# Kernel optimization log

Measured on AMD Instinct MI355X. Metric: run time of the kernel, lower is better.

The kernel has to match this reference:

```python
import jax, jax.numpy as jnp
import numpy as np

N_U, N_V = 8000, 8000
E_U, E_V = 128000, 128000
ND, ED, T = 40, 10, 3


def _lin(key, out_d, in_d):
    k1, k2 = jax.random.split(key)
    s = 1.0 / np.sqrt(in_d)
    w = jax.random.uniform(k1, (out_d, in_d), minval=-s, maxval=s, dtype=jnp.float32)
    b = jax.random.uniform(k2, (out_d,), minval=-s, maxval=s, dtype=jnp.float32)
    return w, b


def _lstm(key, in_d, h_d):
    ks = jax.random.split(key, 4)
    s = 1.0 / np.sqrt(h_d)
    Wih = jax.random.uniform(ks[0], (4 * h_d, in_d), minval=-s, maxval=s, dtype=jnp.float32)
    Whh = jax.random.uniform(ks[1], (4 * h_d, h_d), minval=-s, maxval=s, dtype=jnp.float32)
    bih = jax.random.uniform(ks[2], (4 * h_d,), minval=-s, maxval=s, dtype=jnp.float32)
    bhh = jax.random.uniform(ks[3], (4 * h_d,), minval=-s, maxval=s, dtype=jnp.float32)
    return Wih, Whh, bih, bhh


def _mp_params(key):
    ks = jax.random.split(key, 2 * T)
    Uw, Ub, Mw, Mb = [], [], [], []
    for k in range(T):
        w, b = _lin(ks[2 * k], ND, 2 * ND + ED); Uw.append(w); Ub.append(b)
        w, b = _lin(ks[2 * k + 1], ND, 2 * ND); Mw.append(w); Mb.append(b)
    return jnp.stack(Uw), jnp.stack(Ub), jnp.stack(Mw), jnp.stack(Mb)


def setup_inputs():
    key = jax.random.key(0)
    ks = jax.random.split(key, 20)
    d = {}
    d["nodes_u"] = jax.random.normal(ks[0], (N_U, ND), jnp.float32)
    d["ei_u"] = jax.random.randint(ks[1], (2, E_U), 0, N_U)
    d["ef_u"] = jax.random.normal(ks[2], (E_U, ED), jnp.float32)
    d["nodes_v"] = jax.random.normal(ks[3], (N_V, ND), jnp.float32)
    d["ei_v"] = jax.random.randint(ks[4], (2, E_V), 0, N_V)
    d["ef_v"] = jax.random.normal(ks[5], (E_V, ED), jnp.float32)
    d["Uw_u"], d["Ub_u"], d["Mw_u"], d["Mb_u"] = _mp_params(ks[6])
    d["Uw_v"], d["Ub_v"], d["Mw_v"], d["Mb_v"] = _mp_params(ks[7])
    d["ls_Wih"], d["ls_Whh"], d["ls_bih"], d["ls_bhh"] = _lstm(ks[8], 2 * ND, ND)
    d["lv_Wih"], d["lv_Whh"], d["lv_bih"], d["lv_bhh"] = _lstm(ks[9], 2 * ND, ND)
    d["gs_Wih"], d["gs_Whh"], d["gs_bih"], d["gs_bhh"] = _lstm(ks[10], 8 * ND, 4 * ND)
    d["gv_Wih"], d["gv_Whh"], d["gv_bih"], d["gv_bhh"] = _lstm(ks[11], 8 * ND, 4 * ND)
    d["w1"], d["b1"] = _lin(ks[12], 360, 16 * ND)
    d["w2"], d["b2"] = _lin(ks[13], 200, 360)
    d["w3"], d["b3"] = _lin(ks[14], 120, 200)
    d["w4"], d["b4"] = _lin(ks[15], 1, 120)
    return d


def _lstm_step(x, h, c, Wih, Whh, bih, bhh):
    # one seq_len=1 step of torch nn.LSTM; gate order i, f, g, o
    gates = x @ Wih.T + h @ Whh.T + bih + bhh
    i, f, g, o = jnp.split(gates, 4, axis=-1)
    c = jax.nn.sigmoid(f) * c + jax.nn.sigmoid(i) * jnp.tanh(g)
    h = jax.nn.sigmoid(o) * jnp.tanh(c)
    return h, c


def _message_passing(h, ei, ef, Uw, Ub, Mw, Mb):
    # vectorized form of the per-node Python loop: messages use the
    # pre-update h each round (the torch code computes all messages first).
    src, dst = ei[0], ei[1]
    n = h.shape[0]
    for k in range(T):
        z = jnp.concatenate([h[src], h[dst], ef], axis=-1)   # [E, 2*ND+ED]
        msg_e = z @ Uw[k].T + Ub[k]                          # [E, ND]
        msg = jax.ops.segment_sum(msg_e, src, num_segments=n)
        h = jax.nn.relu(jnp.concatenate([h, msg], axis=-1) @ Mw[k].T + Mb[k])
    return h


def _set2set_pair(h0, ht, Wih, Whh, bih, bhh, steps=2):
    # set of size 2 ({h_0, h_T}) per node; nodes act as the LSTM batch.
    t = jnp.stack([h0, ht], axis=0)                # [2, n, f]
    n, f = h0.shape
    q_star = jnp.zeros((n, 2 * f), h0.dtype)
    h = jnp.zeros((n, f), h0.dtype)
    c = jnp.zeros((n, f), h0.dtype)
    for _ in range(steps):
        h, c = _lstm_step(q_star, h, c, Wih, Whh, bih, bhh)
        e = jnp.sum(t * h[None], axis=2)           # [2, n]
        a = jax.nn.softmax(e, axis=0)
        r = jnp.sum(a[..., None] * t, axis=0)      # [n, f]
        q_star = jnp.concatenate([h, r], axis=1)
    return q_star                                   # [n, 2f]


def _set2set_pool(x, Wih, Whh, bih, bhh, steps=2):
    # attention pooling over nodes, batch of 1 (the gather set2set).
    n, f = x.shape
    q_star = jnp.zeros((1, 2 * f), x.dtype)
    h = jnp.zeros((1, f), x.dtype)
    c = jnp.zeros((1, f), x.dtype)
    for _ in range(steps):
        h, c = _lstm_step(q_star, h, c, Wih, Whh, bih, bhh)
        a = jax.nn.softmax(x @ h[0])                # [n]
        r = (a[:, None] * x).sum(axis=0, keepdims=True)
        q_star = jnp.concatenate([h, r], axis=1)
    return q_star                                    # [1, 2f]


def reference(nodes_u, ei_u, ef_u, nodes_v, ei_v, ef_v,
              Uw_u, Ub_u, Mw_u, Mb_u, Uw_v, Ub_v, Mw_v, Mb_v,
              ls_Wih, ls_Whh, ls_bih, ls_bhh,
              lv_Wih, lv_Whh, lv_bih, lv_bhh,
              gs_Wih, gs_Whh, gs_bih, gs_bhh,
              gv_Wih, gv_Whh, gv_bih, gv_bhh,
              w1, b1, w2, b2, w3, b3, w4, b4):
    hu_t = _message_passing(nodes_u, ei_u, ef_u, Uw_u, Ub_u, Mw_u, Mb_u)
    hv_t = _message_passing(nodes_v, ei_v, ef_v, Uw_v, Ub_v, Mw_v, Mb_v)
    gu = _set2set_pair(nodes_u, hu_t, ls_Wih, ls_Whh, ls_bih, ls_bhh)  # [n, 2*ND]
    gv = _set2set_pair(nodes_v, hv_t, lv_Wih, lv_Whh, lv_bih, lv_bhh)  # [m, 2*ND]
    interaction = gu @ gv.T                          # [n, m]
    im2 = jnp.tanh(interaction)
    u_after = im2 @ gv                               # [n, 2*ND]
    v_after = im2.T @ gu                             # [m, 2*ND]
    cu = _set2set_pool(jnp.concatenate([u_after, gu], 1), gs_Wih, gs_Whh, gs_bih, gs_bhh)
    cv = _set2set_pool(jnp.concatenate([v_after, gv], 1), gv_Wih, gv_Whh, gv_bih, gv_bhh)
    x = jnp.concatenate([cu, cv], axis=1)            # [1, 16*ND]
    x = jax.nn.relu(x @ w1.T + b1)
    x = jax.nn.relu(x @ w2.T + b2)
    x = jax.nn.relu(x @ w3.T + b3)
    x = x @ w4.T + b4                                # [1, 1]
    return (x, interaction)
```

## Files before the change

kernel.cpp:

```cpp
#include <hip/hip_runtime.h>
#include <cstdint>
#include <cstddef>

#define NN 8000
#define NE 128000
#define NDv 40
#define EDv 10

typedef __attribute__((ext_vector_type(8))) short short8v;
typedef __attribute__((ext_vector_type(4))) float f32x4;

__device__ __forceinline__ float rcp_fast(float x) { return __builtin_amdgcn_rcpf(x); }
__device__ __forceinline__ float sigm(float x) { return rcp_fast(1.f + __expf(-x)); }
__device__ __forceinline__ float ftanh(float x) {
    float e = __expf(2.f * x);
    return 1.f - 2.f * rcp_fast(e + 1.f);
}
__device__ __forceinline__ short f2bf(float x) {
    unsigned u = __builtin_bit_cast(unsigned, x);
    u += 0x7fffu + ((u >> 16) & 1u);
    return (short)(u >> 16);
}
__device__ __forceinline__ float wsum(float v) {
    for (int o = 32; o; o >>= 1) v += __shfl_down(v, o);
    return v;
}
__device__ __forceinline__ float wmax(float v) {
    for (int o = 32; o; o >>= 1) v = fmaxf(v, __shfl_down(v, o));
    return v;
}


__global__ __launch_bounds__(256) void csr_deg2_kernel(const int* __restrict__ ei_u, const int* __restrict__ ei_v,
                                                       int* __restrict__ deg_u, int* __restrict__ deg_v) {
    const int* ei = blockIdx.y ? ei_v : ei_u;
    int* deg = blockIdx.y ? deg_v : deg_u;
    int e = blockIdx.x * 256 + threadIdx.x;
    if (e < NE) atomicAdd(&deg[ei[e]], 1);
}

__global__ __launch_bounds__(256) void sef2_kernel(const int* __restrict__ ei_u, const int* __restrict__ ei_v,
                                                   const float* __restrict__ ef_u, const float* __restrict__ ef_v,
                                                   float* __restrict__ sef_u, float* __restrict__ sef_v) {
    const int* ei = blockIdx.y ? ei_v : ei_u;
    const float* ef = blockIdx.y ? ef_v : ef_u;
    float* sef = blockIdx.y ? sef_v : sef_u;
    int t = blockIdx.x * 256 + threadIdx.x;
    int e = t / EDv, k = t % EDv;
    atomicAdd(&sef[ei[e] * EDv + k], ef[t]);
}

__global__ __launch_bounds__(64) void csr_scan2_kernel(const int* __restrict__ deg_u, const int* __restrict__ deg_v,
                                                       int* __restrict__ off_u, int* __restrict__ off_v,
                                                       int* __restrict__ woff_u, int* __restrict__ woff_v) {
    const int* deg = blockIdx.x ? deg_v : deg_u;
    int* off = blockIdx.x ? off_v : off_u;
    int* woff = blockIdx.x ? woff_v : woff_u;
    int l = threadIdx.x;
    int base = l * 125;
    int s = 0;
    for (int i = 0; i < 125; ++i) s += deg[base + i];
    int pre = s;
    for (int o = 1; o < 64; o <<= 1) { int t = __shfl_up(pre, o); if (l >= o) pre += t; }
    pre -= s;
    int run = pre;
    for (int i = 0; i < 125; ++i) {
        off[base + i] = run; woff[base + i] = run;
        run += deg[base + i];
    }
    if (l == 63) off[NN] = run;
}

__global__ __launch_bounds__(256) void csr_fill2_kernel(const int* __restrict__ ei_u, const int* __restrict__ ei_v,
                                                        int* __restrict__ woff_u, int* __restrict__ woff_v,
                                                        int* __restrict__ dl_u, int* __restrict__ dl_v) {
    const int* ei = blockIdx.y ? ei_v : ei_u;
    int* woff = blockIdx.y ? woff_v : woff_u;
    int* dlist = blockIdx.y ? dl_v : dl_u;
    int e = blockIdx.x * 256 + threadIdx.x;
    if (e < NE) { int p = atomicAdd(&woff[ei[e]], 1); dlist[p] = ei[NE + e]; }
}


__global__ __launch_bounds__(256) void node_proj2_kernel(const float* __restrict__ h_u, const float* __restrict__ h_v,
                                                         const float* __restrict__ Uw_u, const float* __restrict__ Uw_v,
                                                         float* __restrict__ A_u, float* __restrict__ B_u,
                                                         float* __restrict__ A_v, float* __restrict__ B_v) {
    const float* h = blockIdx.y ? h_v : h_u;
    const float* Uw = blockIdx.y ? Uw_v : Uw_u;
    float* A = blockIdx.y ? A_v : A_u;
    float* B = blockIdx.y ? B_v : B_u;
    __shared__ float W[40][81];
    int tid = threadIdx.x;
    for (int s = tid; s < 3200; s += 256) W[s / 80][s % 80] = Uw[(s / 80) * 90 + (s % 80)];
    __syncthreads();
    int t = blockIdx.x * 256 + tid;
    int n = t / NDv, i = t % NDv;
    float hreg[40];
    const float* hr = h + n * NDv;
#pragma unroll
    for (int k4 = 0; k4 < 10; ++k4) {
        float4 v = *reinterpret_cast<const float4*>(hr + k4 * 4);
        hreg[k4 * 4 + 0] = v.x; hreg[k4 * 4 + 1] = v.y; hreg[k4 * 4 + 2] = v.z; hreg[k4 * 4 + 3] = v.w;
    }
    float a = 0.f, b = 0.f;
#pragma unroll
    for (int k = 0; k < NDv; ++k) { a += W[i][k] * hreg[k]; b += W[i][40 + k] * hreg[k]; }
    A[t] = a; B[t] = b;
}

__global__ __launch_bounds__(320) void mp_round2_kernel(
    const int* __restrict__ off_u, const int* __restrict__ dl_u, const float* __restrict__ sef_u,
    const float* __restrict__ UwE_u, const float* __restrict__ Ub_u,
    const float* __restrict__ Mw_u, const float* __restrict__ Mb_u, const float* __restrict__ UwN_u,
    const float* __restrict__ h_u, const float* __restrict__ A_u, const float* __restrict__ B_u,
    float* __restrict__ hout_u, float* __restrict__ Ao_u, float* __restrict__ Bo_u,
    const int* __restrict__ off_v, const int* __restrict__ dl_v, const float* __restrict__ sef_v,
    const float* __restrict__ UwE_v, const float* __restrict__ Ub_v,
    const float* __restrict__ Mw_v, const float* __restrict__ Mb_v, const float* __restrict__ UwN_v,
    const float* __restrict__ h_v, const float* __restrict__ A_v, const float* __restrict__ B_v,
    float* __restrict__ hout_v, float* __restrict__ Ao_v, float* __restrict__ Bo_v,
    int has_next) {
    const int* off = blockIdx.y ? off_v : off_u;
    const int* dlist = blockIdx.y ? dl_v : dl_u;
    const float* sef = blockIdx.y ? sef_v : sef_u;
    const float* UwE = blockIdx.y ? UwE_v : UwE_u;
    const float* Ub = blockIdx.y ? Ub_v : Ub_u;
    const float* Mw = blockIdx.y ? Mw_v : Mw_u;
    const float* Mb = blockIdx.y ? Mb_v : Mb_u;
    const float* UwN = blockIdx.y ? UwN_v : UwN_u;
    const float* h = blockIdx.y ? h_v : h_u;
    const float* A = blockIdx.y ? A_v : A_u;
    const float* B = blockIdx.y ? B_v : B_u;
    float* hout = blockIdx.y ? hout_v : hout_u;
    float* Ao = blockIdx.y ? Ao_v : Ao_u;
    float* Bo = blockIdx.y ? Bo_v : Bo_u;

    __shared__ float WM[40][81];
    __shared__ float WU[40][81];
    __shared__ float msgS[8][40];
    __shared__ float hS[8][41];
    __shared__ float houtS[8][41];

    int tid = threadIdx.x;
    for (int s = tid; s < 3200; s += 320) WM[s / 80][s % 80] = Mw[s];
    if (has_next)
        for (int s = tid; s < 3200; s += 320) WU[s / 80][s % 80] = UwN[(s / 80) * 90 + (s % 80)];
    int ln = tid / NDv, i = tid % NDv;
    int n = blockIdx.x * 8 + ln;
    int t = n * NDv + i;
    hS[ln][i] = h[t];

    const float* we = UwE + i * 90 + 80;
    const float* se = sef + n * EDv;
    int p0 = off[n], p1 = off[n + 1];
    float acc = (float)(p1 - p0) * (A[t] + Ub[i]);
#pragma unroll
    for (int k = 0; k < EDv; ++k) acc += we[k] * se[k];
    for (int p = p0; p < p1; ++p) acc += B[dlist[p] * NDv + i];
    msgS[ln][i] = acc;
    __syncthreads();

    float a2 = Mb[i];
#pragma unroll
    for (int k = 0; k < NDv; ++k) a2 += WM[i][k] * hS[ln][k];
#pragma unroll
    for (int k = 0; k < NDv; ++k) a2 += WM[i][40 + k] * msgS[ln][k];
    float ho = fmaxf(a2, 0.f);
    hout[t] = ho;
    if (has_next) {
        houtS[ln][i] = ho;
        __syncthreads();
        float a = 0.f, b = 0.f;
#pragma unroll
        for (int k = 0; k < NDv; ++k) { float hv = houtS[ln][k]; a += WU[i][k] * hv; b += WU[i][40 + k] * hv; }
        Ao[t] = a; Bo[t] = b;
    }
}


__global__ __launch_bounds__(64) void s2s_init2_kernel(const float* __restrict__ bih_u, const float* __restrict__ bhh_u,
                                                       const float* __restrict__ bih_v, const float* __restrict__ bhh_v,
                                                       float* __restrict__ h1_u, float* __restrict__ c1_u,
                                                       float* __restrict__ h1_v, float* __restrict__ c1_v) {
    const float* bih = blockIdx.y ? bih_v : bih_u;
    const float* bhh = blockIdx.y ? bhh_v : bhh_u;
    float* h1 = blockIdx.y ? h1_v : h1_u;
    float* c1 = blockIdx.y ? c1_v : c1_u;
    int i = threadIdx.x;
    if (i < 40) {
        float gi = bih[i] + bhh[i];
        float gg = bih[80 + i] + bhh[80 + i];
        float go = bih[120 + i] + bhh[120 + i];
        float c = sigm(gi) * ftanh(gg);
        c1[i] = c;
        h1[i] = sigm(go) * ftanh(c);
    }
}

__global__ __launch_bounds__(256) void s2s_step0_kernel(const float* __restrict__ h0_u, const float* __restrict__ ht_u,
                                                        const float* __restrict__ h1_u, float* __restrict__ q_u,
                                                        float* __restrict__ rT_u,
                                                        const float* __restrict__ h0_v, const float* __restrict__ ht_v,
                                                        const float* __restrict__ h1_v, float* __restrict__ q_v,
                                                        float* __restrict__ rT_v) {
    const float* h0 = blockIdx.y ? h0_v : h0_u;
    const float* ht = blockIdx.y ? ht_v : ht_u;
    const float* h1 = blockIdx.y ? h1_v : h1_u;
    float* q = blockIdx.y ? q_v : q_u;
    float* rT = blockIdx.y ? rT_v : rT_u;
    int tid = threadIdx.x;
    int nl = tid >> 2, lg = tid & 3;
    int n = blockIdx.x * 64 + nl;
    float h0r[10], htr[10];
    float e0 = 0.f, e1 = 0.f;
#pragma unroll
    for (int k = 0; k < 10; ++k) {
        int i = lg * 10 + k;
        h0r[k] = h0[n * 40 + i];
        htr[k] = ht[n * 40 + i];
        float hv = h1[i];
        e0 += h0r[k] * hv;
        e1 += htr[k] * hv;
    }
    e0 += __shfl_xor(e0, 1); e0 += __shfl_xor(e0, 2);
    e1 += __shfl_xor(e1, 1); e1 += __shfl_xor(e1, 2);
    float m = fmaxf(e0, e1);
    float p0 = __expf(e0 - m), p1 = __expf(e1 - m);
    float inv = rcp_fast(p0 + p1);
    float a0 = p0 * inv, a1 = p1 * inv;
#pragma unroll
    for (int k = 0; k < 10; ++k) {
        int i = lg * 10 + k;
        float r = a0 * h0r[k] + a1 * htr[k];
        q[n * 80 + i] = h1[i];
        q[n * 80 + 40 + i] = r;
        rT[i * NN + n] = r;
    }
}

__global__ __launch_bounds__(64) void s2s_base2_kernel(const float* __restrict__ Wih_u, const float* __restrict__ Whh_u,
                                                       const float* __restrict__ bih_u, const float* __restrict__ bhh_u,
                                                       const float* __restrict__ h1_u,
                                                       const float* __restrict__ Wih_v, const float* __restrict__ Whh_v,
                                                       const float* __restrict__ bih_v, const float* __restrict__ bhh_v,
                                                       const float* __restrict__ h1_v,
                                                       float* __restrict__ base2) {
    const float* Wih = blockIdx.y ? Wih_v : Wih_u;
    const float* Whh = blockIdx.y ? Whh_v : Whh_u;
    const float* bih = blockIdx.y ? bih_v : bih_u;
    const float* bhh = blockIdx.y ? bhh_v : bhh_u;
    const float* h1 = blockIdx.y ? h1_v : h1_u;
    int j = blockIdx.x;
    int lane = threadIdx.x;
    float p = 0.f;
    if (lane < 40) p = (Wih[j * 80 + lane] + Whh[j * 40 + lane]) * h1[lane];
    p = wsum(p);
    if (lane == 0) base2[blockIdx.y * 160 + j] = p + bih[j] + bhh[j];
}

__global__ __launch_bounds__(256) void s2s_gates1_kernel(const float* __restrict__ rT_u, const float* __restrict__ Wih_u,
                                                         float* __restrict__ gT_u,
                                                         const float* __restrict__ rT_v, const float* __restrict__ Wih_v,
                                                         float* __restrict__ gT_v,
                                                         const float* __restrict__ base2) {
    const float* rT = blockIdx.y ? rT_v : rT_u;
    const float* Wih = blockIdx.y ? Wih_v : Wih_u;
    float* gatesT = blockIdx.y ? gT_v : gT_u;
    const float* base = base2 + blockIdx.y * 160;
    int t = blockIdx.x * 256 + threadIdx.x;
    int n = t % NN;
    int jg = t / NN;
    float rr[40];
#pragma unroll
    for (int k = 0; k < 40; ++k) rr[k] = rT[k * NN + n];
#pragma unroll
    for (int jj = 0; jj < 8; ++jj) {
        int j = jg * 8 + jj;
        const float* wi = Wih + j * 80 + 40;
        float acc = base[j];
#pragma unroll
        for (int k = 0; k < 40; ++k) acc += wi[k] * rr[k];
        gatesT[j * NN + n] = acc;
    }
}

__global__ __launch_bounds__(256) void s2s_upd1_kernel(const float* __restrict__ gT_u, const float* __restrict__ h0_u,
                                                       const float* __restrict__ ht_u, const float* __restrict__ c1_u,
                                                       float* __restrict__ q_u,
                                                       const float* __restrict__ gT_v, const float* __restrict__ h0_v,
                                                       const float* __restrict__ ht_v, const float* __restrict__ c1_v,
                                                       float* __restrict__ q_v) {
    const float* gT = blockIdx.y ? gT_v : gT_u;
    const float* h0 = blockIdx.y ? h0_v : h0_u;
    const float* ht = blockIdx.y ? ht_v : ht_u;
    const float* c1 = blockIdx.y ? c1_v : c1_u;
    float* q = blockIdx.y ? q_v : q_u;
    int tid = threadIdx.x;
    int nl = tid >> 2, lg = tid & 3;
    int n = blockIdx.x * 64 + nl;
    float h0r[10], htr[10], hnr[10];
    float e0 = 0.f, e1 = 0.f;
#pragma unroll
    for (int k = 0; k < 10; ++k) {
        int i = lg * 10 + k;
        float gi = gT[i * NN + n];
        float gf = gT[(40 + i) * NN + n];
        float gg = gT[(80 + i) * NN + n];
        float go = gT[(120 + i) * NN + n];
        float cn = sigm(gf) * c1[i] + sigm(gi) * ftanh(gg);
        float hn = sigm(go) * ftanh(cn);
        hnr[k] = hn;
        h0r[k] = h0[n * 40 + i];
        htr[k] = ht[n * 40 + i];
        e0 += h0r[k] * hn;
        e1 += htr[k] * hn;
    }
    e0 += __shfl_xor(e0, 1); e0 += __shfl_xor(e0, 2);
    e1 += __shfl_xor(e1, 1); e1 += __shfl_xor(e1, 2);
    float m = fmaxf(e0, e1);
    float p0 = __expf(e0 - m), p1 = __expf(e1 - m);
    float inv = rcp_fast(p0 + p1);
    float a0 = p0 * inv, a1 = p1 * inv;
#pragma unroll
    for (int k = 0; k < 10; ++k) {
        int i = lg * 10 + k;
        q[n * 80 + i] = hnr[k];
        q[n * 80 + 40 + i] = a0 * h0r[k] + a1 * htr[k];
    }
}


__global__ __launch_bounds__(256) void cast_all_kernel(const float* __restrict__ gu, const float* __restrict__ gv,
                                                       short* __restrict__ ouT, short* __restrict__ ovT,
                                                       short* __restrict__ oub, short* __restrict__ ovb,
                                                       float* __restrict__ qTu, float* __restrict__ qTv) {
    const float* g = blockIdx.y ? gv : gu;
    if (blockIdx.x < 2500) {
        short* o = blockIdx.y ? ovT : ouT;
        float* qT = blockIdx.y ? qTv : qTu;
        int t = blockIdx.x * 256 + threadIdx.x;
        int m = t % NN, f = t / NN;
        float val = g[m * 80 + f];
        o[t] = f2bf(val);
        qT[t] = val;
    } else {
        short* o = blockIdx.y ? ovb : oub;
        int t = (blockIdx.x - 2500) * 256 + threadIdx.x;
        int m = t / 96, k = t % 96;
        o[t] = (k < 80) ? f2bf(g[m * 80 + k]) : (short)0;
    }
}


__global__ __launch_bounds__(256, 2) void fused_kernel(const short* __restrict__ gub, const short* __restrict__ gvb,
                                                       const short* __restrict__ guT, const short* __restrict__ gvT,
                                                       float* __restrict__ inter,
                                                       float* __restrict__ uafT, float* __restrict__ vafT) {
    __shared__ short P[4][16][72];
    const short* Xb; const short* Yb; const short* YT; float* afT;
    bool storeI = (blockIdx.z == 0);
    if (storeI) { Xb = gub; Yb = gvb; YT = gvT; afT = uafT; }
    else        { Xb = gvb; Yb = gub; YT = guT; afT = vafT; }
    int tid = threadIdx.x;
    int w = tid >> 6, l = tid & 63;
    int lrow = l & 15, lk = l >> 4;
    int x0 = blockIdx.x * 64;
    int it0 = (125 * blockIdx.y) >> 1;
    int it1 = (125 * (blockIdx.y + 1)) >> 1;
    short8v a_x[3];
    const short* arow = Xb + (size_t)(x0 + w * 16 + lrow) * 96 + lk * 8;
#pragma unroll
    for (int ks = 0; ks < 3; ++ks) a_x[ks] = *reinterpret_cast<const short8v*>(arow + ks * 32);
    const short* ybase = Yb + (size_t)lrow * 96 + lk * 8;

    f32x4 acc[5] = {};
    short8v bc[12], bn[12];
#pragma unroll
    for (int i = 0; i < 12; ++i) {
        int ks = i >> 2, nt = i & 3;
        bc[i] = *reinterpret_cast<const short8v*>(ybase + (size_t)(it0 * 64 + nt * 16) * 96 + ks * 32);
    }
    for (int it = it0; it < it1; ++it) {
        int k0 = it * 64;
        if (it + 1 < it1) {
#pragma unroll
            for (int i = 0; i < 12; ++i) {
                int ks = i >> 2, nt = i & 3;
                bn[i] = *reinterpret_cast<const short8v*>(ybase + (size_t)(k0 + 64 + nt * 16) * 96 + ks * 32);
            }
        }
        short8v byt[10];
#pragma unroll
        for (int ks2 = 0; ks2 < 2; ++ks2)
#pragma unroll
            for (int ft = 0; ft < 5; ++ft)
                byt[ks2 * 5 + ft] = *reinterpret_cast<const short8v*>(YT + (size_t)(ft * 16 + lrow) * NN + k0 + ks2 * 32 + lk * 8);
        f32x4 accI[4] = {};
#pragma unroll
        for (int ks = 0; ks < 3; ++ks)
#pragma unroll
            for (int nt = 0; nt < 4; ++nt)
                accI[nt] = __builtin_amdgcn_mfma_f32_16x16x32_bf16(a_x[ks], bc[ks * 4 + nt], accI[nt], 0, 0, 0);
#pragma unroll
        for (int nt = 0; nt < 4; ++nt)
#pragma unroll
            for (int r = 0; r < 4; ++r)
                P[w][lk * 4 + r][nt * 16 + lrow] = f2bf(ftanh(accI[nt][r]));
#pragma unroll
        for (int ks2 = 0; ks2 < 2; ++ks2) {
            short8v ap = *reinterpret_cast<const short8v*>(&P[w][lrow][ks2 * 32 + lk * 8]);
#pragma unroll
            for (int ft = 0; ft < 5; ++ft)
                acc[ft] = __builtin_amdgcn_mfma_f32_16x16x32_bf16(ap, byt[ks2 * 5 + ft], acc[ft], 0, 0, 0);
        }
        if (storeI) {
#pragma unroll
            for (int nt = 0; nt < 4; ++nt)
#pragma unroll
                for (int r = 0; r < 4; ++r)
                    inter[(size_t)(x0 + w * 16 + lk * 4 + r) * NN + (k0 + nt * 16 + lrow)] = accI[nt][r];
        }
#pragma unroll
        for (int i = 0; i < 12; ++i) bc[i] = bn[i];
    }
    int xout = x0 + w * 16 + lk * 4;
#pragma unroll
    for (int ft = 0; ft < 5; ++ft)
#pragma unroll
        for (int r = 0; r < 4; ++r)
            atomicAdd(&afT[(size_t)(ft * 16 + lrow) * NN + xout + r], acc[ft][r]);
}


__global__ __launch_bounds__(256) void pool_init2_kernel(const float* __restrict__ bih_u, const float* __restrict__ bhh_u,
                                                         const float* __restrict__ bih_v, const float* __restrict__ bhh_v,
                                                         float* __restrict__ ph_u, float* __restrict__ pc_u,
                                                         float* __restrict__ pq_u,
                                                         float* __restrict__ ph_v, float* __restrict__ pc_v,
                                                         float* __restrict__ pq_v) {
    const float* bih = blockIdx.y ? bih_v : bih_u;
    const float* bhh = blockIdx.y ? bhh_v : bhh_u;
    float* ph = blockIdx.y ? ph_v : ph_u;
    float* pc = blockIdx.y ? pc_v : pc_u;
    float* pq = blockIdx.y ? pq_v : pq_u;
    int i = threadIdx.x;
    if (i < 160) {
        float gi = bih[i] + bhh[i];
        float gg = bih[320 + i] + bhh[320 + i];
        float go = bih[480 + i] + bhh[480 + i];
        float c = sigm(gi) * ftanh(gg);
        pc[i] = c;
        float h = sigm(go) * ftanh(c);
        ph[i] = h;
        pq[i] = h;
    }
}

__global__ __launch_bounds__(64) void gates_pool2_kernel(const float* __restrict__ Wih_u, const float* __restrict__ Whh_u,
                                                         const float* __restrict__ bih_u, const float* __restrict__ bhh_u,
                                                         const float* __restrict__ q_u, const float* __restrict__ h_u,
                                                         const float* __restrict__ Wih_v, const float* __restrict__ Whh_v,
                                                         const float* __restrict__ bih_v, const float* __restrict__ bhh_v,
                                                         const float* __restrict__ q_v, const float* __restrict__ h_v,
                                                         float* __restrict__ gts2) {
    const float* Wih = blockIdx.y ? Wih_v : Wih_u;
    const float* Whh = blockIdx.y ? Whh_v : Whh_u;
    const float* bih = blockIdx.y ? bih_v : bih_u;
    const float* bhh = blockIdx.y ? bhh_v : bhh_u;
    const float* q = blockIdx.y ? q_v : q_u;
    const float* h = blockIdx.y ? h_v : h_u;
    float* gts = gts2 + blockIdx.y * 640;
    int j = blockIdx.x;
    int lane = threadIdx.x;
    const float* wi = Wih + j * 320;
    const float* wh = Whh + j * 160;
    float p = 0.f;
#pragma unroll
    for (int k4 = 0; k4 < 5; ++k4) { int k = lane + k4 * 64; p += wi[k] * q[k]; }
#pragma unroll
    for (int k4 = 0; k4 < 3; ++k4) { int k = lane + k4 * 64; if (k < 160) p += wh[k] * h[k]; }
    p = wsum(p);
    if (lane == 0) gts[j] = p + bih[j] + bhh[j];
}

__global__ __launch_bounds__(256) void pool_point2_kernel(const float* __restrict__ gts2,
                                                          float* __restrict__ h_u, float* __restrict__ c_u,
                                                          float* __restrict__ q_u,
                                                          float* __restrict__ h_v, float* __restrict__ c_v,
                                                          float* __restrict__ q_v) {
    const float* gts = gts2 + blockIdx.y * 640;
    float* h = blockIdx.y ? h_v : h_u;
    float* c = blockIdx.y ? c_v : c_u;
    float* q = blockIdx.y ? q_v : q_u;
    int tid = threadIdx.x;
    if (tid < 160) {
        float cn = sigm(gts[160 + tid]) * c[tid] + sigm(gts[tid]) * ftanh(gts[320 + tid]);
        c[tid] = cn;
        float hn = sigm(gts[480 + tid]) * ftanh(cn);
        h[tid] = hn;
        q[tid] = hn;
    }
}

__global__ __launch_bounds__(256) void pool_scores2_kernel(const float* __restrict__ uafT, const float* __restrict__ qTu,
                                                           const float* __restrict__ h_u, float* __restrict__ sc_u,
                                                           const float* __restrict__ vafT, const float* __restrict__ qTv,
                                                           const float* __restrict__ h_v, float* __restrict__ sc_v,
                                                           float* __restrict__ pmax2) {
    const float* afT = blockIdx.y ? vafT : uafT;
    const float* qT = blockIdx.y ? qTv : qTu;
    const float* h = blockIdx.y ? h_v : h_u;
    float* scores = blockIdx.y ? sc_v : sc_u;
    float* pmax = pmax2 + blockIdx.y * 32;
    int tid = threadIdx.x;
    int n = blockIdx.x * 256 + tid;
    float s = -3.4e38f;
    if (n < NN) {
        float acc = 0.f;
#pragma unroll 8
        for (int k = 0; k < 80; ++k) acc += afT[k * NN + n] * h[k];
#pragma unroll 8
        for (int k = 0; k < 80; ++k) acc += qT[k * NN + n] * h[80 + k];
        scores[n] = acc;
        s = acc;
    }
    __shared__ float red[4];
    float m = wmax(s);
    if ((tid & 63) == 0) red[tid >> 6] = m;
    __syncthreads();
    if (tid == 0) pmax[blockIdx.x] = fmaxf(fmaxf(red[0], red[1]), fmaxf(red[2], red[3]));
}

__global__ __launch_bounds__(256) void pool_r2_kernel(const float* __restrict__ uafT, const float* __restrict__ qTu,
                                                      const float* __restrict__ sc_u,
                                                      const float* __restrict__ vafT, const float* __restrict__ qTv,
                                                      const float* __restrict__ sc_v,
                                                      const float* __restrict__ pmax2,
                                                      float* __restrict__ pq_u, float* __restrict__ pq_v) {
    const float* afT = blockIdx.y ? vafT : uafT;
    const float* qT = blockIdx.y ? qTv : qTu;
    const float* scores = blockIdx.y ? sc_v : sc_u;
    float* q = blockIdx.y ? pq_v : pq_u;
    const float* pmax = pmax2 + blockIdx.y * 32;
    int f = blockIdx.x;
    int tid = threadIdx.x;
    __shared__ float smax;
    __shared__ float reda[4], redd[4];
    if (tid < 64) {
        float m = (tid < 32) ? pmax[tid] : -3.4e38f;
        m = wmax(m);
        if (tid == 0) smax = m;
    }
    __syncthreads();
    float m = smax;
    const float* x = (f < 80) ? (afT + (size_t)f * NN) : (qT + (size_t)(f - 80) * NN);
    float acc = 0.f, den = 0.f;
    for (int n = tid; n < NN; n += 256) { float e = __expf(scores[n] - m); den += e; acc += e * x[n]; }
    float wa = wsum(acc), wd = wsum(den);
    if ((tid & 63) == 0) { reda[tid >> 6] = wa; redd[tid >> 6] = wd; }
    __syncthreads();
    if (tid == 0) {
        float A = reda[0] + reda[1] + reda[2] + reda[3];
        float D = redd[0] + redd[1] + redd[2] + redd[3];
        q[160 + f] = A * rcp_fast(D);
    }
}


__global__ __launch_bounds__(64) void gemv_kernel(const float* __restrict__ W, const float* __restrict__ b,
                                                  const float* __restrict__ x, float* __restrict__ y,
                                                  int K, int relu) {
    int j = blockIdx.x;
    int lane = threadIdx.x;
    const float* w = W + (size_t)j * K;
    float p = 0.f;
    for (int k = lane; k < K; k += 64) p += w[k] * x[k];
    p = wsum(p);
    if (lane == 0) {
        p += b[j];
        y[j] = relu ? fmaxf(p, 0.f) : p;
    }
}


extern "C" void kernel_launch(void* const* d_in, const int* in_sizes, int n_in,
                              void* d_out, int out_size, void* d_ws, size_t ws_size,
                              hipStream_t stream) {
    const float* nodes_u = (const float*)d_in[0];
    const int* ei_u = (const int*)d_in[1];
    const float* ef_u = (const float*)d_in[2];
    const float* nodes_v = (const float*)d_in[3];
    const int* ei_v = (const int*)d_in[4];
    const float* ef_v = (const float*)d_in[5];
    const float* Uw_u = (const float*)d_in[6];
    const float* Ub_u = (const float*)d_in[7];
    const float* Mw_u = (const float*)d_in[8];
    const float* Mb_u = (const float*)d_in[9];
    const float* Uw_v = (const float*)d_in[10];
    const float* Ub_v = (const float*)d_in[11];
    const float* Mw_v = (const float*)d_in[12];
    const float* Mb_v = (const float*)d_in[13];
    const float* lsWih = (const float*)d_in[14];
    const float* lsWhh = (const float*)d_in[15];
    const float* lsbih = (const float*)d_in[16];
    const float* lsbhh = (const float*)d_in[17];
    const float* lvWih = (const float*)d_in[18];
    const float* lvWhh = (const float*)d_in[19];
    const float* lvbih = (const float*)d_in[20];
    const float* lvbhh = (const float*)d_in[21];
    const float* gsWih = (const float*)d_in[22];
    const float* gsWhh = (const float*)d_in[23];
    const float* gsbih = (const float*)d_in[24];
    const float* gsbhh = (const float*)d_in[25];
    const float* gvWih = (const float*)d_in[26];
    const float* gvWhh = (const float*)d_in[27];
    const float* gvbih = (const float*)d_in[28];
    const float* gvbhh = (const float*)d_in[29];
    const float* w1 = (const float*)d_in[30];
    const float* b1 = (const float*)d_in[31];
    const float* w2 = (const float*)d_in[32];
    const float* b2 = (const float*)d_in[33];
    const float* w3 = (const float*)d_in[34];
    const float* b3 = (const float*)d_in[35];
    const float* w4 = (const float*)d_in[36];
    const float* b4 = (const float*)d_in[37];

    float* ws = (float*)d_ws;
    float* hA_u = ws + 0;
    float* hB_u = ws + 320000;
    float* hA_v = ws + 640000;
    float* hB_v = ws + 960000;
    float* A0_u = ws + 1600000;
    float* B0_u = ws + 1920000;
    float* q_u  = ws + 2240000;
    float* q_v  = ws + 2880000;
    float* A1_u = ws + 2240000;
    float* B1_u = ws + 2560000;
    float* A1_v = ws + 2880000;
    float* B1_v = ws + 3200000;
    float* sef_u = ws + 4160000;
    float* sef_v = ws + 4240000;
    float* gT_u = ws + 4160000;
    float* gT_v = ws + 5440000;
    float* uafT = ws + 5440000;
    float* vafT = ws + 6080000;
    float* rT_u = ws + 1600000;
    float* rT_v = ws + 1920000;
    float* qT_u = ws + 1600000;
    float* qT_v = ws + 2240000;
    float* sc_u = ws + 6720000;
    float* sc_v = ws + 6728000;
    float* pmax2 = ws + 6736000;
    float* pq_u = ws + 6736080;
    float* pq_v = ws + 6736400;
    float* ph_u = ws + 6736720;
    float* pc_u = ws + 6736880;
    float* ph_v = ws + 6737040;
    float* pc_v = ws + 6737200;
    float* pgts2 = ws + 6737360;
    float* mx1  = ws + 6738640;
    float* mx2  = ws + 6739000;
    float* mx3  = ws + 6739200;
    float* h1_u = ws + 6739320;
    float* c1_u = ws + 6739360;
    float* h1_v = ws + 6739400;
    float* c1_v = ws + 6739440;
    float* base2 = ws + 6739480;
    int* ioff_u   = (int*)(ws + 6740000);
    int* idlist_u = (int*)(ws + 6748064);
    int* ioff_v   = (int*)(ws + 6876064);
    int* idlist_v = (int*)(ws + 6884128);
    int* iwoff_u  = (int*)(ws + 7012128);
    int* ideg_u   = (int*)(ws + 7020192);
    int* iwoff_v  = (int*)(ws + 7028256);
    int* ideg_v   = (int*)(ws + 7036320);
    float* A0_v = ws + 7339536;
    float* B0_v = ws + 7659536;

    short* guT = (short*)(ws + 0);
    short* gvT = (short*)(ws + 320000);
    short* gub = (short*)(ws + 640000);
    short* gvb = (short*)(ws + 1024000);

    float* out = (float*)d_out;
    float* inter = out + 1;

    hipMemsetAsync(ideg_u, 0, (7044384 - 7020192) * sizeof(int), stream);
    hipMemsetAsync(sef_u, 0, 2 * NN * EDv * sizeof(float), stream);
    csr_deg2_kernel<<<dim3(500, 2), 256, 0, stream>>>(ei_u, ei_v, ideg_u, ideg_v);
    csr_scan2_kernel<<<2, 64, 0, stream>>>(ideg_u, ideg_v, ioff_u, ioff_v, iwoff_u, iwoff_v);
    csr_fill2_kernel<<<dim3(500, 2), 256, 0, stream>>>(ei_u, ei_v, iwoff_u, iwoff_v, idlist_u, idlist_v);
    sef2_kernel<<<dim3(5000, 2), 256, 0, stream>>>(ei_u, ei_v, ef_u, ef_v, sef_u, sef_v);

    node_proj2_kernel<<<dim3(1250, 2), 256, 0, stream>>>(nodes_u, nodes_v, Uw_u, Uw_v, A0_u, B0_u, A0_v, B0_v);
    mp_round2_kernel<<<dim3(1000, 2), 320, 0, stream>>>(
        ioff_u, idlist_u, sef_u, Uw_u, Ub_u, Mw_u, Mb_u, Uw_u + 3600,
        nodes_u, A0_u, B0_u, hA_u, A1_u, B1_u,
        ioff_v, idlist_v, sef_v, Uw_v, Ub_v, Mw_v, Mb_v, Uw_v + 3600,
        nodes_v, A0_v, B0_v, hA_v, A1_v, B1_v, 1);
    mp_round2_kernel<<<dim3(1000, 2), 320, 0, stream>>>(
        ioff_u, idlist_u, sef_u, Uw_u + 3600, Ub_u + 40, Mw_u + 3200, Mb_u + 40, Uw_u + 7200,
        hA_u, A1_u, B1_u, hB_u, A0_u, B0_u,
        ioff_v, idlist_v, sef_v, Uw_v + 3600, Ub_v + 40, Mw_v + 3200, Mb_v + 40, Uw_v + 7200,
        hA_v, A1_v, B1_v, hB_v, A0_v, B0_v, 1);
    mp_round2_kernel<<<dim3(1000, 2), 320, 0, stream>>>(
        ioff_u, idlist_u, sef_u, Uw_u + 7200, Ub_u + 80, Mw_u + 6400, Mb_u + 80, nullptr,
        hB_u, A0_u, B0_u, hA_u, nullptr, nullptr,
        ioff_v, idlist_v, sef_v, Uw_v + 7200, Ub_v + 80, Mw_v + 6400, Mb_v + 80, nullptr,
        hB_v, A0_v, B0_v, hA_v, nullptr, nullptr, 0);

    s2s_init2_kernel<<<dim3(1, 2), 64, 0, stream>>>(lsbih, lsbhh, lvbih, lvbhh, h1_u, c1_u, h1_v, c1_v);
    s2s_step0_kernel<<<dim3(125, 2), 256, 0, stream>>>(nodes_u, hA_u, h1_u, q_u, rT_u,
                                                       nodes_v, hA_v, h1_v, q_v, rT_v);
    s2s_base2_kernel<<<dim3(160, 2), 64, 0, stream>>>(lsWih, lsWhh, lsbih, lsbhh, h1_u,
                                                      lvWih, lvWhh, lvbih, lvbhh, h1_v, base2);
    s2s_gates1_kernel<<<dim3(625, 2), 256, 0, stream>>>(rT_u, lsWih, gT_u, rT_v, lvWih, gT_v, base2);
    s2s_upd1_kernel<<<dim3(125, 2), 256, 0, stream>>>(gT_u, nodes_u, hA_u, c1_u, q_u,
                                                      gT_v, nodes_v, hA_v, c1_v, q_v);

    cast_all_kernel<<<dim3(5500, 2), 256, 0, stream>>>(q_u, q_v, guT, gvT, gub, gvb, qT_u, qT_v);

    hipMemsetAsync(uafT, 0, 1280000 * sizeof(float), stream);
    fused_kernel<<<dim3(125, 2, 2), 256, 0, stream>>>(gub, gvb, guT, gvT, inter, uafT, vafT);

    pool_init2_kernel<<<dim3(1, 2), 256, 0, stream>>>(gsbih, gsbhh, gvbih, gvbhh,
                                                      ph_u, pc_u, pq_u, ph_v, pc_v, pq_v);
    pool_scores2_kernel<<<dim3(32, 2), 256, 0, stream>>>(uafT, qT_u, ph_u, sc_u, vafT, qT_v, ph_v, sc_v, pmax2);
    pool_r2_kernel<<<dim3(160, 2), 256, 0, stream>>>(uafT, qT_u, sc_u, vafT, qT_v, sc_v, pmax2, pq_u, pq_v);
    gates_pool2_kernel<<<dim3(640, 2), 64, 0, stream>>>(gsWih, gsWhh, gsbih, gsbhh, pq_u, ph_u,
                                                        gvWih, gvWhh, gvbih, gvbhh, pq_v, ph_v, pgts2);
    pool_point2_kernel<<<dim3(1, 2), 256, 0, stream>>>(pgts2, ph_u, pc_u, pq_u, ph_v, pc_v, pq_v);
    pool_scores2_kernel<<<dim3(32, 2), 256, 0, stream>>>(uafT, qT_u, ph_u, sc_u, vafT, qT_v, ph_v, sc_v, pmax2);
    pool_r2_kernel<<<dim3(160, 2), 256, 0, stream>>>(uafT, qT_u, sc_u, vafT, qT_v, sc_v, pmax2, pq_u, pq_v);

    gemv_kernel<<<360, 64, 0, stream>>>(w1, b1, pq_u, mx1, 640, 1);
    gemv_kernel<<<200, 64, 0, stream>>>(w2, b2, mx1, mx2, 360, 1);
    gemv_kernel<<<120, 64, 0, stream>>>(w3, b3, mx2, mx3, 200, 1);
    gemv_kernel<<<1, 64, 0, stream>>>(w4, b4, mx3, out, 120, 0);
}
```

Before: 635.6 us.

## Fuse set2set gate GEMV into LSTM update, enlarge MP blocks, unsplit fused grid

```diff
diff --git a/kernel.cpp b/kernel.cpp
--- a/kernel.cpp
+++ b/kernel.cpp
@@ -109,7 +109,7 @@
     A[t] = a; B[t] = b;
 }
 
-__global__ __launch_bounds__(320) void mp_round2_kernel(
+__global__ __launch_bounds__(640) void mp_round2_kernel(
     const int* __restrict__ off_u, const int* __restrict__ dl_u, const float* __restrict__ sef_u,
     const float* __restrict__ UwE_u, const float* __restrict__ Ub_u,
     const float* __restrict__ Mw_u, const float* __restrict__ Mb_u, const float* __restrict__ UwN_u,
@@ -138,16 +138,16 @@
 
     __shared__ float WM[40][81];
     __shared__ float WU[40][81];
-    __shared__ float msgS[8][40];
-    __shared__ float hS[8][41];
-    __shared__ float houtS[8][41];
+    __shared__ float msgS[16][40];
+    __shared__ float hS[16][41];
+    __shared__ float houtS[16][41];
 
     int tid = threadIdx.x;
-    for (int s = tid; s < 3200; s += 320) WM[s / 80][s % 80] = Mw[s];
+    for (int s = tid; s < 3200; s += 640) WM[s / 80][s % 80] = Mw[s];
     if (has_next)
-        for (int s = tid; s < 3200; s += 320) WU[s / 80][s % 80] = UwN[(s / 80) * 90 + (s % 80)];
+        for (int s = tid; s < 3200; s += 640) WU[s / 80][s % 80] = UwN[(s / 80) * 90 + (s % 80)];
     int ln = tid / NDv, i = tid % NDv;
-    int n = blockIdx.x * 8 + ln;
+    int n = blockIdx.x * 16 + ln;
     int t = n * NDv + i;
     hS[ln][i] = h[t];
 
@@ -259,57 +259,45 @@
     if (lane == 0) base2[blockIdx.y * 160 + j] = p + bih[j] + bhh[j];
 }
 
-__global__ __launch_bounds__(256) void s2s_gates1_kernel(const float* __restrict__ rT_u, const float* __restrict__ Wih_u,
-                                                         float* __restrict__ gT_u,
-                                                         const float* __restrict__ rT_v, const float* __restrict__ Wih_v,
-                                                         float* __restrict__ gT_v,
-                                                         const float* __restrict__ base2) {
+__global__ __launch_bounds__(256) void s2s_step1_kernel(const float* __restrict__ rT_u, const float* __restrict__ Wih_u,
+                                                        const float* __restrict__ h0_u, const float* __restrict__ ht_u,
+                                                        const float* __restrict__ c1_u, float* __restrict__ q_u,
+                                                        const float* __restrict__ rT_v, const float* __restrict__ Wih_v,
+                                                        const float* __restrict__ h0_v, const float* __restrict__ ht_v,
+                                                        const float* __restrict__ c1_v, float* __restrict__ q_v,
+                                                        const float* __restrict__ base2) {
     const float* rT = blockIdx.y ? rT_v : rT_u;
     const float* Wih = blockIdx.y ? Wih_v : Wih_u;
-    float* gatesT = blockIdx.y ? gT_v : gT_u;
-    const float* base = base2 + blockIdx.y * 160;
-    int t = blockIdx.x * 256 + threadIdx.x;
-    int n = t % NN;
-    int jg = t / NN;
-    float rr[40];
-#pragma unroll
-    for (int k = 0; k < 40; ++k) rr[k] = rT[k * NN + n];
-#pragma unroll
-    for (int jj = 0; jj < 8; ++jj) {
-        int j = jg * 8 + jj;
-        const float* wi = Wih + j * 80 + 40;
-        float acc = base[j];
-#pragma unroll
-        for (int k = 0; k < 40; ++k) acc += wi[k] * rr[k];
-        gatesT[j * NN + n] = acc;
-    }
-}
-
-__global__ __launch_bounds__(256) void s2s_upd1_kernel(const float* __restrict__ gT_u, const float* __restrict__ h0_u,
-                                                       const float* __restrict__ ht_u, const float* __restrict__ c1_u,
-                                                       float* __restrict__ q_u,
-                                                       const float* __restrict__ gT_v, const float* __restrict__ h0_v,
-                                                       const float* __restrict__ ht_v, const float* __restrict__ c1_v,
-                                                       float* __restrict__ q_v) {
-    const float* gT = blockIdx.y ? gT_v : gT_u;
     const float* h0 = blockIdx.y ? h0_v : h0_u;
     const float* ht = blockIdx.y ? ht_v : ht_u;
     const float* c1 = blockIdx.y ? c1_v : c1_u;
     float* q = blockIdx.y ? q_v : q_u;
+    const float* base = base2 + blockIdx.y * 160;
     int tid = threadIdx.x;
     int nl = tid >> 2, lg = tid & 3;
     int n = blockIdx.x * 64 + nl;
+    float rr[40];
+#pragma unroll
+    for (int k = 0; k < 40; ++k) rr[k] = rT[k * NN + n];
+    float g[40];
+#pragma unroll
+    for (int gq = 0; gq < 4; ++gq)
+#pragma unroll
+        for (int k = 0; k < 10; ++k) {
+            int j = gq * 40 + lg * 10 + k;
+            const float* wi = Wih + j * 80 + 40;
+            float acc = base[j];
+#pragma unroll
+            for (int kk = 0; kk < 40; ++kk) acc += wi[kk] * rr[kk];
+            g[gq * 10 + k] = acc;
+        }
     float h0r[10], htr[10], hnr[10];
     float e0 = 0.f, e1 = 0.f;
 #pragma unroll
     for (int k = 0; k < 10; ++k) {
         int i = lg * 10 + k;
-        float gi = gT[i * NN + n];
-        float gf = gT[(40 + i) * NN + n];
-        float gg = gT[(80 + i) * NN + n];
-        float go = gT[(120 + i) * NN + n];
-        float cn = sigm(gf) * c1[i] + sigm(gi) * ftanh(gg);
-        float hn = sigm(go) * ftanh(cn);
+        float cn = sigm(g[10 + k]) * c1[i] + sigm(g[k]) * ftanh(g[20 + k]);
+        float hn = sigm(g[30 + k]) * ftanh(cn);
         hnr[k] = hn;
         h0r[k] = h0[n * 40 + i];
         htr[k] = ht[n * 40 + i];
@@ -366,8 +354,7 @@
     int w = tid >> 6, l = tid & 63;
     int lrow = l & 15, lk = l >> 4;
     int x0 = blockIdx.x * 64;
-    int it0 = (125 * blockIdx.y) >> 1;
-    int it1 = (125 * (blockIdx.y + 1)) >> 1;
+    const int it0 = 0, it1 = 125;
     short8v a_x[3];
     const short* arow = Xb + (size_t)(x0 + w * 16 + lrow) * 96 + lk * 8;
 #pragma unroll
@@ -641,8 +628,6 @@
     float* B1_v = ws + 3200000;
     float* sef_u = ws + 4160000;
     float* sef_v = ws + 4240000;
-    float* gT_u = ws + 4160000;
-    float* gT_v = ws + 5440000;
     float* uafT = ws + 5440000;
     float* vafT = ws + 6080000;
     float* rT_u = ws + 1600000;
@@ -694,17 +679,17 @@
     sef2_kernel<<<dim3(5000, 2), 256, 0, stream>>>(ei_u, ei_v, ef_u, ef_v, sef_u, sef_v);
 
     node_proj2_kernel<<<dim3(1250, 2), 256, 0, stream>>>(nodes_u, nodes_v, Uw_u, Uw_v, A0_u, B0_u, A0_v, B0_v);
-    mp_round2_kernel<<<dim3(1000, 2), 320, 0, stream>>>(
+    mp_round2_kernel<<<dim3(500, 2), 640, 0, stream>>>(
         ioff_u, idlist_u, sef_u, Uw_u, Ub_u, Mw_u, Mb_u, Uw_u + 3600,
         nodes_u, A0_u, B0_u, hA_u, A1_u, B1_u,
         ioff_v, idlist_v, sef_v, Uw_v, Ub_v, Mw_v, Mb_v, Uw_v + 3600,
         nodes_v, A0_v, B0_v, hA_v, A1_v, B1_v, 1);
-    mp_round2_kernel<<<dim3(1000, 2), 320, 0, stream>>>(
+    mp_round2_kernel<<<dim3(500, 2), 640, 0, stream>>>(
         ioff_u, idlist_u, sef_u, Uw_u + 3600, Ub_u + 40, Mw_u + 3200, Mb_u + 40, Uw_u + 7200,
         hA_u, A1_u, B1_u, hB_u, A0_u, B0_u,
         ioff_v, idlist_v, sef_v, Uw_v + 3600, Ub_v + 40, Mw_v + 3200, Mb_v + 40, Uw_v + 7200,
         hA_v, A1_v, B1_v, hB_v, A0_v, B0_v, 1);
-    mp_round2_kernel<<<dim3(1000, 2), 320, 0, stream>>>(
+    mp_round2_kernel<<<dim3(500, 2), 640, 0, stream>>>(
         ioff_u, idlist_u, sef_u, Uw_u + 7200, Ub_u + 80, Mw_u + 6400, Mb_u + 80, nullptr,
         hB_u, A0_u, B0_u, hA_u, nullptr, nullptr,
         ioff_v, idlist_v, sef_v, Uw_v + 7200, Ub_v + 80, Mw_v + 6400, Mb_v + 80, nullptr,
@@ -715,14 +700,13 @@
                                                        nodes_v, hA_v, h1_v, q_v, rT_v);
     s2s_base2_kernel<<<dim3(160, 2), 64, 0, stream>>>(lsWih, lsWhh, lsbih, lsbhh, h1_u,
                                                       lvWih, lvWhh, lvbih, lvbhh, h1_v, base2);
-    s2s_gates1_kernel<<<dim3(625, 2), 256, 0, stream>>>(rT_u, lsWih, gT_u, rT_v, lvWih, gT_v, base2);
-    s2s_upd1_kernel<<<dim3(125, 2), 256, 0, stream>>>(gT_u, nodes_u, hA_u, c1_u, q_u,
-                                                      gT_v, nodes_v, hA_v, c1_v, q_v);
+    s2s_step1_kernel<<<dim3(125, 2), 256, 0, stream>>>(rT_u, lsWih, nodes_u, hA_u, c1_u, q_u,
+                                                       rT_v, lvWih, nodes_v, hA_v, c1_v, q_v, base2);
 
     cast_all_kernel<<<dim3(5500, 2), 256, 0, stream>>>(q_u, q_v, guT, gvT, gub, gvb, qT_u, qT_v);
 
     hipMemsetAsync(uafT, 0, 1280000 * sizeof(float), stream);
-    fused_kernel<<<dim3(125, 2, 2), 256, 0, stream>>>(gub, gvb, guT, gvT, inter, uafT, vafT);
+    fused_kernel<<<dim3(125, 1, 2), 256, 0, stream>>>(gub, gvb, guT, gvT, inter, uafT, vafT);
 
     pool_init2_kernel<<<dim3(1, 2), 256, 0, stream>>>(gsbih, gsbhh, gvbih, gvbhh,
                                                       ph_u, pc_u, pq_u, ph_v, pc_v, pq_v);
```

New measurement: 644.3 us. About the same (+1.4%).
